# Kernel tuning notes

Measured on AMD Instinct MI355X. Metric: run time of the kernel, lower is better.

Reference implementation:

```python
import jax, jax.numpy as jnp
import numpy as np

N_HEADS = 12

def setup_inputs() -> dict:
    key = jax.random.key(0)
    ks = jax.random.split(key, 3)
    B, C, T = 4, 768, 2048
    x = jax.random.normal(ks[0], (B, C, T), dtype=jnp.float32)
    mask = jnp.ones((B, 1, 1, T), dtype=jnp.int32)  # all valid; masked_fill where mask==0
    Wqkv = jax.random.normal(ks[1], (3 * C, C), dtype=jnp.float32) * 0.02
    bqkv = jnp.zeros((3 * C,), dtype=jnp.float32)
    Wout = jax.random.normal(ks[2], (C, C), dtype=jnp.float32) * 0.02
    bout = jnp.zeros((C,), dtype=jnp.float32)
    return {"x": x, "mask": mask, "Wqkv": Wqkv, "bqkv": bqkv, "Wout": Wout, "bout": bout}


def reference(x, mask, Wqkv, bqkv, Wout, bout):
    B, C, T = x.shape
    H = N_HEADS
    d = C // H
    scale = 1.0 / jnp.sqrt(jnp.asarray(d, x.dtype))
    # 1x1 Conv1d == per-timestep matmul over channels
    qkv = jnp.einsum('oc,bct->bot', Wqkv, x) + bqkv[None, :, None]  # [B,3C,T]
    # channel dim splits as [3, H, d] per the torch view(B,3,H,d,T)
    qkv = qkv.reshape(B, 3, H, d, T).transpose(0, 1, 2, 4, 3)       # [B,3,H,T,d]
    q, k, v = qkv[:, 0], qkv[:, 1], qkv[:, 2]
    score = jnp.einsum('bhtd,bhsd->bhts', q, k) * scale             # [B,H,T,T]
    score = jnp.where(mask == 0, jnp.asarray(-10000.0, score.dtype), score)
    attn = jax.nn.softmax(score, axis=-1)  # dropout: eval mode (identity)
    o = jnp.einsum('bhts,bhsd->bhtd', attn, v)                      # [B,H,T,d]
    o = o.transpose(0, 1, 3, 2).reshape(B, C, T)                    # [B,C,T]
    return jnp.einsum('oc,bct->bot', Wout, o) + bout[None, :, None]
```

## Files before the change

kernel.cpp:

```cpp
#include <hip/hip_runtime.h>
#include <hip/hip_bf16.h>
#include <stdint.h>

#define B_   4
#define C_   768
#define T_   2048
#define H_   12
#define D_   64
#define O3_  2304

typedef __attribute__((ext_vector_type(4))) float f32x4;
typedef __attribute__((ext_vector_type(8))) short bf16x8;

__device__ __forceinline__ unsigned short f2bf(float f) {
  union { float f; unsigned int u; } v; v.f = f;
  unsigned int r = v.u + 0x7fffu + ((v.u >> 16) & 1u);
  return (unsigned short)(r >> 16);
}

__device__ __forceinline__ unsigned int pack2bf(float a, float b) {
  __hip_bfloat162 h2 = __float22bfloat162_rn(make_float2(a, b));
  union { __hip_bfloat162 h; unsigned int u; } cv; cv.h = h2;
  return cv.u;
}

__device__ __forceinline__ float fexp2(float x) {
#if __has_builtin(__builtin_amdgcn_exp2f)
  return __builtin_amdgcn_exp2f(x);
#else
  return exp2f(x);
#endif
}

__device__ __forceinline__ void async16(const void* g, void* lds) {
#if __has_builtin(__builtin_amdgcn_global_load_lds)
  __builtin_amdgcn_global_load_lds((const __attribute__((address_space(1))) void*)g,
                                   (__attribute__((address_space(3))) void*)lds, 16, 0, 0);
#else
  int lane = threadIdx.x & 63;
  *((uint4*)((char*)lds + lane * 16)) = *((const uint4*)g);
#endif
}


__global__ void cvt_f32_bf16(const float* __restrict__ in,
                             unsigned short* __restrict__ out, int n4) {
  int i = blockIdx.x * 256 + threadIdx.x;
  if (i < n4) {
    float4 f = ((const float4*)in)[i];
    ushort4 o;
    o.x = f2bf(f.x); o.y = f2bf(f.y); o.z = f2bf(f.z); o.w = f2bf(f.w);
    ((ushort4*)out)[i] = o;
  }
}

__global__ void make_bias(const int* __restrict__ mask, float* __restrict__ mbias, int n) {
  int i = blockIdx.x * 256 + threadIdx.x;
  if (i < n) mbias[i] = (mask[i] == 0) ? -14426.950408f : 0.0f;
}

__global__ void transpose_x(const float* __restrict__ x,
                            unsigned short* __restrict__ xT) {
  __shared__ unsigned short tile[32][33];
  int b = blockIdx.z;
  int c0 = blockIdx.y * 32;
  int t0 = blockIdx.x * 32;
  int tid = threadIdx.x;
  {
    int cl = tid >> 3;
    int tl = (tid & 7) * 4;
    float4 f = *(const float4*)(x + ((size_t)b * C_ + c0 + cl) * T_ + t0 + tl);
    tile[tl + 0][cl] = f2bf(f.x);
    tile[tl + 1][cl] = f2bf(f.y);
    tile[tl + 2][cl] = f2bf(f.z);
    tile[tl + 3][cl] = f2bf(f.w);
  }
  __syncthreads();
  {
    int tl = tid >> 3;
    int cl = (tid & 7) * 4;
    ushort4 o;
    o.x = tile[tl][cl + 0]; o.y = tile[tl][cl + 1];
    o.z = tile[tl][cl + 2]; o.w = tile[tl][cl + 3];
    *(ushort4*)(xT + ((size_t)b * T_ + t0 + tl) * C_ + c0 + cl) = o;
  }
}

__global__ __launch_bounds__(256)
void gemm_qkv(const unsigned short* __restrict__ xT,
              const unsigned short* __restrict__ W1,
              const float* __restrict__ bqkv,
              unsigned short* __restrict__ Qb,
              unsigned short* __restrict__ Kb,
              unsigned short* __restrict__ Vb) {
  __shared__ unsigned short sA[2][128 * 32];
  __shared__ unsigned short sB[2][128 * 32];

  const int b   = blockIdx.z;
  const int o0  = blockIdx.y * 128;
  const int t0  = blockIdx.x * 128;
  const int tid = threadIdx.x;
  const int wave = tid >> 6, lane = tid & 63;
  const int q = lane >> 4, ln = lane & 15;
  const int tw = wave >> 1, ow = wave & 1;

  const unsigned short* Ax = xT + (size_t)b * T_ * C_;
  const int srow = lane >> 2;
  const int scol = (lane & 3) * 8;

  const f32x4 ZERO = {0.f, 0.f, 0.f, 0.f};
  f32x4 acc[4][4];
#pragma unroll
  for (int mi = 0; mi < 4; ++mi)
#pragma unroll
    for (int ni = 0; ni < 4; ++ni) acc[mi][ni] = ZERO;

#pragma unroll
  for (int j = 0; j < 2; ++j) {
    const int chunk = wave * 2 + j;
    const int row = chunk * 16 + srow;
    async16(Ax + (size_t)(t0 + row) * C_ + scol, &sA[0][chunk * 512]);
    async16(W1 + (size_t)(o0 + row) * C_ + scol, &sB[0][chunk * 512]);
  }

  for (int i = 0; i < 24; ++i) {
    const int buf = i & 1;
    __syncthreads();
    if (i < 23) {
      const int k0 = (i + 1) * 32;
#pragma unroll
      for (int j = 0; j < 2; ++j) {
        const int chunk = wave * 2 + j;
        const int row = chunk * 16 + srow;
        async16(Ax + (size_t)(t0 + row) * C_ + k0 + scol, &sA[buf ^ 1][chunk * 512]);
        async16(W1 + (size_t)(o0 + row) * C_ + k0 + scol, &sB[buf ^ 1][chunk * 512]);
      }
    }

    bf16x8 aF[4], bF[4];
#pragma unroll
    for (int mi = 0; mi < 4; ++mi)
      aF[mi] = *(const bf16x8*)(&sA[buf][(tw * 64 + mi * 16 + ln) * 32 + q * 8]);
#pragma unroll
    for (int ni = 0; ni < 4; ++ni)
      bF[ni] = *(const bf16x8*)(&sB[buf][(ow * 64 + ni * 16 + ln) * 32 + q * 8]);
#pragma unroll
    for (int mi = 0; mi < 4; ++mi)
#pragma unroll
      for (int ni = 0; ni < 4; ++ni)
        acc[mi][ni] = __builtin_amdgcn_mfma_f32_16x16x32_bf16(aF[mi], bF[ni], acc[mi][ni], 0, 0, 0);
  }

  const float QSCL = 0.125f * 1.44269504f;
#pragma unroll
  for (int ni = 0; ni < 4; ++ni) {
    const int o = o0 + ow * 64 + ni * 16 + ln;
    const float bias = bqkv[o];
    const int which = o / C_;
    const int rem = o - which * C_;
    const int bh = b * H_ + (rem >> 6);
    const int dd = rem & 63;
#pragma unroll
    for (int mi = 0; mi < 4; ++mi) {
      const int tb = t0 + tw * 64 + mi * 16 + q * 4;
      f32x4 v = acc[mi][ni];
      if (which == 0) {
#pragma unroll
        for (int r = 0; r < 4; ++r)
          Qb[((size_t)bh * T_ + tb + r) * D_ + dd] = f2bf((v[r] + bias) * QSCL);
      } else if (which == 1) {
#pragma unroll
        for (int r = 0; r < 4; ++r) {
          const int s = tb + r;
          const int cp = (dd >> 3) ^ (s & 7);
          Kb[((size_t)bh * T_ + s) * 64 + (cp << 3) + (dd & 7)] = f2bf(v[r] + bias);
        }
      } else {
        const int tile = tb >> 6, si = tb & 63;
        const int cp = (si >> 3) ^ (dd & 7);
        ushort4 pk;
        pk.x = f2bf(v[0] + bias);
        pk.y = f2bf(v[1] + bias);
        pk.z = f2bf(v[2] + bias);
        pk.w = f2bf(v[3] + bias);
        *(ushort4*)(Vb + (((size_t)bh * 32 + tile) * 64 + dd) * 64 + (cp << 3) + (si & 7)) = pk;
      }
    }
  }
}

__global__ __launch_bounds__(128, 2)
void attn(const unsigned short* __restrict__ Qb,
          const unsigned short* __restrict__ Kb,
          const unsigned short* __restrict__ Vb,
          const float* __restrict__ mbias,
          unsigned short* __restrict__ Ob) {
  __shared__ unsigned short sK[2][64 * 64];
  __shared__ unsigned short sV[2][64 * 64];
  __shared__ unsigned short sP[2][64 * 80];

  const int id = blockIdx.x;
  const int bh = id % 48;
  const int tblk = id / 48;
  const int b = bh / H_, h = bh % H_;
  const int tid = threadIdx.x, wave = tid >> 6, lane = tid & 63;
  const int q = lane >> 4, ln = lane & 15;
  const int t0w = tblk * 128 + wave * 64;
  unsigned short* sPw = &sP[wave][0];

  bf16x8 Qa[4][2];
#pragma unroll
  for (int tt = 0; tt < 4; ++tt) {
    const unsigned short* qrow = Qb + ((size_t)bh * T_ + t0w + tt * 16 + ln) * D_;
    Qa[tt][0] = *(const bf16x8*)(qrow + q * 8);
    Qa[tt][1] = *(const bf16x8*)(qrow + 32 + q * 8);
  }

  const f32x4 ZERO = {0.f, 0.f, 0.f, 0.f};
  f32x4 Oacc[4][4];
  f32x4 lacc[4];
#pragma unroll
  for (int dt = 0; dt < 4; ++dt)
#pragma unroll
    for (int tt = 0; tt < 4; ++tt) Oacc[dt][tt] = ZERO;
#pragma unroll
  for (int tt = 0; tt < 4; ++tt) lacc[tt] = ZERO;

  const short one_s = (ln == 0) ? (short)0x3F80 : (short)0;
  bf16x8 ones;
#pragma unroll
  for (int j = 0; j < 8; ++j) ones[j] = one_s;

  const unsigned short* gK = Kb + (size_t)bh * T_ * 64;
  const unsigned short* gV = Vb + (size_t)bh * 32 * 4096;

#pragma unroll
  for (int j = 0; j < 4; ++j) {
    const int chunk = j * 2 + wave;
    async16(gK + chunk * 512 + lane * 8, &sK[0][chunk * 512]);
    async16(gV + chunk * 512 + lane * 8, &sV[0][chunk * 512]);
  }

  for (int it = 0; it < 32; ++it) {
    const int buf = it & 1;
    __syncthreads();
    if (it < 31) {
      const unsigned short* k = gK + (it + 1) * 4096;
      const unsigned short* v = gV + (it + 1) * 4096;
#pragma unroll
      for (int j = 0; j < 4; ++j) {
        const int chunk = j * 2 + wave;
        async16(k + chunk * 512 + lane * 8, &sK[buf ^ 1][chunk * 512]);
        async16(v + chunk * 512 + lane * 8, &sV[buf ^ 1][chunk * 512]);
      }
    }

    const int s0 = it * 64;
    const float bvl = mbias[b * T_ + s0 + lane];
    const bool anymask = (__ballot(bvl != 0.0f) != 0ull);
    const unsigned short* sKc = &sK[buf][0];
    const unsigned short* sVc = &sV[buf][0];

#pragma unroll
    for (int sb = 0; sb < 4; ++sb) {
      const unsigned short* krow = sKc + (sb * 16 + ln) * 64;
      bf16x8 kf0 = *(const bf16x8*)(krow + ((q ^ (ln & 7)) << 3));
      bf16x8 kf1 = *(const bf16x8*)(krow + (((4 + q) ^ (ln & 7)) << 3));
      f32x4 bb = ZERO;
      if (anymask) bb = *(const f32x4*)(mbias + b * T_ + s0 + sb * 16 + q * 4);
#pragma unroll
      for (int tt = 0; tt < 4; ++tt) {
        f32x4 p0 = __builtin_amdgcn_mfma_f32_16x16x32_bf16(kf0, Qa[tt][0], ZERO, 0, 0, 0);
        f32x4 sc = __builtin_amdgcn_mfma_f32_16x16x32_bf16(kf1, Qa[tt][1], p0, 0, 0, 0);
        if (anymask) {
#pragma unroll
          for (int r = 0; r < 4; ++r) sc[r] += bb[r];
        }
        uint2 w;
        w.x = pack2bf(fexp2(sc[0]), fexp2(sc[1]));
        w.y = pack2bf(fexp2(sc[2]), fexp2(sc[3]));
        *(uint2*)(sPw + (tt * 16 + ln) * 80 + sb * 16 + q * 4) = w;
      }
    }

#pragma unroll
    for (int c = 0; c < 2; ++c) {
      bf16x8 vf[4];
#pragma unroll
      for (int dt = 0; dt < 4; ++dt)
        vf[dt] = *(const bf16x8*)(sVc + (dt * 16 + ln) * 64 +
                                  (((c * 4 + q) ^ (ln & 7)) << 3));
#pragma unroll
      for (int tt = 0; tt < 4; ++tt) {
        bf16x8 pf = *(const bf16x8*)(sPw + (tt * 16 + ln) * 80 + c * 32 + q * 8);
        lacc[tt] = __builtin_amdgcn_mfma_f32_16x16x32_bf16(ones, pf, lacc[tt], 0, 0, 0);
#pragma unroll
        for (int dt = 0; dt < 4; ++dt)
          Oacc[dt][tt] = __builtin_amdgcn_mfma_f32_16x16x32_bf16(vf[dt], pf, Oacc[dt][tt], 0, 0, 0);
      }
    }
  }

#pragma unroll
  for (int tt = 0; tt < 4; ++tt) {
    const float lv = __shfl(lacc[tt][0], ln, 64);
    const float inv = 1.0f / lv;
    const int t = t0w + tt * 16 + ln;
#pragma unroll
    for (int dt = 0; dt < 4; ++dt) {
      ushort4 pk;
      pk.x = f2bf(Oacc[dt][tt][0] * inv);
      pk.y = f2bf(Oacc[dt][tt][1] * inv);
      pk.z = f2bf(Oacc[dt][tt][2] * inv);
      pk.w = f2bf(Oacc[dt][tt][3] * inv);
      *(ushort4*)(Ob + ((size_t)b * T_ + t) * C_ + h * D_ + dt * 16 + q * 4) = pk;
    }
  }
}

__global__ __launch_bounds__(256)
void gemm_out(const unsigned short* __restrict__ Ob,
              const unsigned short* __restrict__ W2,
              const float* __restrict__ bout,
              float* __restrict__ out) {
  __shared__ unsigned short sA[2][128 * 32];
  __shared__ unsigned short sB[2][128 * 32];

  const int b   = blockIdx.z;
  const int o0  = blockIdx.y * 128;
  const int t0  = blockIdx.x * 128;
  const int tid = threadIdx.x;
  const int wave = tid >> 6, lane = tid & 63;
  const int q = lane >> 4, ln = lane & 15;
  const int tw = wave >> 1, ow = wave & 1;

  const unsigned short* Bo = Ob + (size_t)b * T_ * C_;
  const int srow = lane >> 2;
  const int scol = (lane & 3) * 8;

  const f32x4 ZERO = {0.f, 0.f, 0.f, 0.f};
  f32x4 acc[4][4];
#pragma unroll
  for (int mi = 0; mi < 4; ++mi)
#pragma unroll
    for (int ni = 0; ni < 4; ++ni) acc[mi][ni] = ZERO;

#pragma unroll
  for (int j = 0; j < 2; ++j) {
    const int chunk = wave * 2 + j;
    const int row = chunk * 16 + srow;
    async16(W2 + (size_t)(o0 + row) * C_ + scol, &sA[0][chunk * 512]);
    async16(Bo + (size_t)(t0 + row) * C_ + scol, &sB[0][chunk * 512]);
  }

  for (int i = 0; i < 24; ++i) {
    const int buf = i & 1;
    __syncthreads();
    if (i < 23) {
      const int k0 = (i + 1) * 32;
#pragma unroll
      for (int j = 0; j < 2; ++j) {
        const int chunk = wave * 2 + j;
        const int row = chunk * 16 + srow;
        async16(W2 + (size_t)(o0 + row) * C_ + k0 + scol, &sA[buf ^ 1][chunk * 512]);
        async16(Bo + (size_t)(t0 + row) * C_ + k0 + scol, &sB[buf ^ 1][chunk * 512]);
      }
    }

    bf16x8 aF[4], bF[4];
#pragma unroll
    for (int mi = 0; mi < 4; ++mi)
      aF[mi] = *(const bf16x8*)(&sA[buf][(tw * 64 + mi * 16 + ln) * 32 + q * 8]);
#pragma unroll
    for (int ni = 0; ni < 4; ++ni)
      bF[ni] = *(const bf16x8*)(&sB[buf][(ow * 64 + ni * 16 + ln) * 32 + q * 8]);
#pragma unroll
    for (int mi = 0; mi < 4; ++mi)
#pragma unroll
      for (int ni = 0; ni < 4; ++ni)
        acc[mi][ni] = __builtin_amdgcn_mfma_f32_16x16x32_bf16(aF[mi], bF[ni], acc[mi][ni], 0, 0, 0);
  }

#pragma unroll
  for (int mi = 0; mi < 4; ++mi) {
    const int ob = o0 + tw * 64 + mi * 16 + q * 4;
#pragma unroll
    for (int ni = 0; ni < 4; ++ni) {
      const int t = t0 + ow * 64 + ni * 16 + ln;
      f32x4 v = acc[mi][ni];
#pragma unroll
      for (int r = 0; r < 4; ++r)
        out[((size_t)b * C_ + ob + r) * T_ + t] = v[r] + bout[ob + r];
    }
  }
}


extern "C" void kernel_launch(void* const* d_in, const int* in_sizes, int n_in,
                              void* d_out, int out_size, void* d_ws, size_t ws_size,
                              hipStream_t stream) {
  (void)in_sizes; (void)n_in; (void)out_size; (void)ws_size;
  const float* x    = (const float*)d_in[0];
  const int*   mask = (const int*)d_in[1];
  const float* Wqkv = (const float*)d_in[2];
  const float* bqkv = (const float*)d_in[3];
  const float* Wout = (const float*)d_in[4];
  const float* bout = (const float*)d_in[5];
  float* out = (float*)d_out;

  const size_t szHead = (size_t)B_ * H_ * T_ * D_;
  const size_t szBTC  = (size_t)B_ * T_ * C_;
  unsigned short* Qb  = (unsigned short*)d_ws;
  unsigned short* Kb  = Qb + szHead;
  unsigned short* Vb  = Kb + szHead;
  unsigned short* Ob  = Vb + szHead;
  unsigned short* xT  = Ob + szBTC;
  unsigned short* W1b = xT + szBTC;
  unsigned short* W2b = W1b + (size_t)O3_ * C_;
  float* mbias        = (float*)(W2b + (size_t)C_ * C_);

  cvt_f32_bf16<<<dim3((O3_ * C_ / 4 + 255) / 256), 256, 0, stream>>>(Wqkv, W1b, O3_ * C_ / 4);
  cvt_f32_bf16<<<dim3((C_ * C_ / 4 + 255) / 256), 256, 0, stream>>>(Wout, W2b, C_ * C_ / 4);
  make_bias<<<dim3((B_ * T_ + 255) / 256), 256, 0, stream>>>(mask, mbias, B_ * T_);
  transpose_x<<<dim3(T_ / 32, C_ / 32, B_), 256, 0, stream>>>(x, xT);
  gemm_qkv<<<dim3(T_ / 128, O3_ / 128, B_), 256, 0, stream>>>(xT, W1b, bqkv, Qb, Kb, Vb);
  attn<<<dim3(768), 128, 0, stream>>>(Qb, Kb, Vb, mbias, Ob);
  gemm_out<<<dim3(T_ / 128, C_ / 128, B_), 256, 0, stream>>>(Ob, W2b, bout, out);
}
```

Before: 257.4 us.

## Split attention key blocks across two wave pairs and reduce partial outputs

After: 238.0 us. -7.5%, faster.

```diff
diff --git a/kernel.cpp b/kernel.cpp
--- a/kernel.cpp
+++ b/kernel.cpp
@@ -189,15 +189,15 @@
   }
 }
 
-__global__ __launch_bounds__(128, 2)
+__global__ __launch_bounds__(256, 3)
 void attn(const unsigned short* __restrict__ Qb,
           const unsigned short* __restrict__ Kb,
           const unsigned short* __restrict__ Vb,
           const float* __restrict__ mbias,
           unsigned short* __restrict__ Ob) {
-  __shared__ unsigned short sK[2][64 * 64];
-  __shared__ unsigned short sV[2][64 * 64];
-  __shared__ unsigned short sP[2][64 * 80];
+  __shared__ __align__(16) char smem[53248];
+  unsigned short* sK0 = (unsigned short*)smem;
+  unsigned short* sV0 = (unsigned short*)(smem + 16384);
 
   const int id = blockIdx.x;
   const int bh = id % 48;
@@ -205,8 +205,9 @@
   const int b = bh / H_, h = bh % H_;
   const int tid = threadIdx.x, wave = tid >> 6, lane = tid & 63;
   const int q = lane >> 4, ln = lane & 15;
-  const int t0w = tblk * 128 + wave * 64;
-  unsigned short* sPw = &sP[wave][0];
+  const int wj = wave & 1, si = wave >> 1;
+  const int t0w = tblk * 128 + wj * 64;
+  unsigned short* sPw = (unsigned short*)(smem + 32768 + wave * 5120);
 
   bf16x8 Qa[4][2];
 #pragma unroll
@@ -235,10 +236,10 @@
   const unsigned short* gV = Vb + (size_t)bh * 32 * 4096;
 
 #pragma unroll
-  for (int j = 0; j < 4; ++j) {
-    const int chunk = j * 2 + wave;
-    async16(gK + chunk * 512 + lane * 8, &sK[0][chunk * 512]);
-    async16(gV + chunk * 512 + lane * 8, &sV[0][chunk * 512]);
+  for (int j = 0; j < 2; ++j) {
+    const int chunk = wave * 2 + j;
+    async16(gK + chunk * 512 + lane * 8, sK0 + chunk * 512);
+    async16(gV + chunk * 512 + lane * 8, sV0 + chunk * 512);
   }
 
   for (int it = 0; it < 32; ++it) {
@@ -247,27 +248,29 @@
     if (it < 31) {
       const unsigned short* k = gK + (it + 1) * 4096;
       const unsigned short* v = gV + (it + 1) * 4096;
-#pragma unroll
-      for (int j = 0; j < 4; ++j) {
-        const int chunk = j * 2 + wave;
-        async16(k + chunk * 512 + lane * 8, &sK[buf ^ 1][chunk * 512]);
-        async16(v + chunk * 512 + lane * 8, &sV[buf ^ 1][chunk * 512]);
+      unsigned short* dK = sK0 + (buf ^ 1) * 4096;
+      unsigned short* dV = sV0 + (buf ^ 1) * 4096;
+#pragma unroll
+      for (int j = 0; j < 2; ++j) {
+        const int chunk = wave * 2 + j;
+        async16(k + chunk * 512 + lane * 8, dK + chunk * 512);
+        async16(v + chunk * 512 + lane * 8, dV + chunk * 512);
       }
     }
 
     const int s0 = it * 64;
     const float bvl = mbias[b * T_ + s0 + lane];
     const bool anymask = (__ballot(bvl != 0.0f) != 0ull);
-    const unsigned short* sKc = &sK[buf][0];
-    const unsigned short* sVc = &sV[buf][0];
-
-#pragma unroll
-    for (int sb = 0; sb < 4; ++sb) {
-      const unsigned short* krow = sKc + (sb * 16 + ln) * 64;
+    const unsigned short* sKc = sK0 + buf * 4096;
+    const unsigned short* sVc = sV0 + buf * 4096;
+
+#pragma unroll
+    for (int sb = 0; sb < 2; ++sb) {
+      const unsigned short* krow = sKc + (si * 32 + sb * 16 + ln) * 64;
       bf16x8 kf0 = *(const bf16x8*)(krow + ((q ^ (ln & 7)) << 3));
       bf16x8 kf1 = *(const bf16x8*)(krow + (((4 + q) ^ (ln & 7)) << 3));
       f32x4 bb = ZERO;
-      if (anymask) bb = *(const f32x4*)(mbias + b * T_ + s0 + sb * 16 + q * 4);
+      if (anymask) bb = *(const f32x4*)(mbias + b * T_ + s0 + si * 32 + sb * 16 + q * 4);
 #pragma unroll
       for (int tt = 0; tt < 4; ++tt) {
         f32x4 p0 = __builtin_amdgcn_mfma_f32_16x16x32_bf16(kf0, Qa[tt][0], ZERO, 0, 0, 0);
@@ -279,41 +282,55 @@
         uint2 w;
         w.x = pack2bf(fexp2(sc[0]), fexp2(sc[1]));
         w.y = pack2bf(fexp2(sc[2]), fexp2(sc[3]));
-        *(uint2*)(sPw + (tt * 16 + ln) * 80 + sb * 16 + q * 4) = w;
-      }
-    }
-
-#pragma unroll
-    for (int c = 0; c < 2; ++c) {
-      bf16x8 vf[4];
+        *(uint2*)(sPw + (tt * 16 + ln) * 40 + sb * 16 + q * 4) = w;
+      }
+    }
+
+    bf16x8 vf[4];
+#pragma unroll
+    for (int dt = 0; dt < 4; ++dt)
+      vf[dt] = *(const bf16x8*)(sVc + (dt * 16 + ln) * 64 +
+                                (((si * 4 + q) ^ (ln & 7)) << 3));
+#pragma unroll
+    for (int tt = 0; tt < 4; ++tt) {
+      bf16x8 pf = *(const bf16x8*)(sPw + (tt * 16 + ln) * 40 + q * 8);
+      lacc[tt] = __builtin_amdgcn_mfma_f32_16x16x32_bf16(ones, pf, lacc[tt], 0, 0, 0);
 #pragma unroll
       for (int dt = 0; dt < 4; ++dt)
-        vf[dt] = *(const bf16x8*)(sVc + (dt * 16 + ln) * 64 +
-                                  (((c * 4 + q) ^ (ln & 7)) << 3));
-#pragma unroll
-      for (int tt = 0; tt < 4; ++tt) {
-        bf16x8 pf = *(const bf16x8*)(sPw + (tt * 16 + ln) * 80 + c * 32 + q * 8);
-        lacc[tt] = __builtin_amdgcn_mfma_f32_16x16x32_bf16(ones, pf, lacc[tt], 0, 0, 0);
-#pragma unroll
-        for (int dt = 0; dt < 4; ++dt)
-          Oacc[dt][tt] = __builtin_amdgcn_mfma_f32_16x16x32_bf16(vf[dt], pf, Oacc[dt][tt], 0, 0, 0);
-      }
-    }
-  }
-
-#pragma unroll
-  for (int tt = 0; tt < 4; ++tt) {
-    const float lv = __shfl(lacc[tt][0], ln, 64);
-    const float inv = 1.0f / lv;
-    const int t = t0w + tt * 16 + ln;
-#pragma unroll
-    for (int dt = 0; dt < 4; ++dt) {
-      ushort4 pk;
-      pk.x = f2bf(Oacc[dt][tt][0] * inv);
-      pk.y = f2bf(Oacc[dt][tt][1] * inv);
-      pk.z = f2bf(Oacc[dt][tt][2] * inv);
-      pk.w = f2bf(Oacc[dt][tt][3] * inv);
-      *(ushort4*)(Ob + ((size_t)b * T_ + t) * C_ + h * D_ + dt * 16 + q * 4) = pk;
+        Oacc[dt][tt] = __builtin_amdgcn_mfma_f32_16x16x32_bf16(vf[dt], pf, Oacc[dt][tt], 0, 0, 0);
+    }
+  }
+
+  __syncthreads();
+  float* fbuf = (float*)smem;
+  float* lbuf = (float*)(smem + 34816);
+  if (si == 1) {
+#pragma unroll
+    for (int tt = 0; tt < 4; ++tt) {
+#pragma unroll
+      for (int dt = 0; dt < 4; ++dt)
+        *(f32x4*)(fbuf + ((size_t)(wj * 64 + tt * 16 + ln)) * 68 + dt * 16 + q * 4) = Oacc[dt][tt];
+      if (q == 0) lbuf[wj * 64 + tt * 16 + ln] = lacc[tt][0];
+    }
+  }
+  __syncthreads();
+  if (si == 0) {
+#pragma unroll
+    for (int tt = 0; tt < 4; ++tt) {
+      const float lv = __shfl(lacc[tt][0], ln, 64) + lbuf[wj * 64 + tt * 16 + ln];
+      const float inv = 1.0f / lv;
+      const int t = t0w + tt * 16 + ln;
+#pragma unroll
+      for (int dt = 0; dt < 4; ++dt) {
+        f32x4 o = Oacc[dt][tt];
+        f32x4 p = *(const f32x4*)(fbuf + ((size_t)(wj * 64 + tt * 16 + ln)) * 68 + dt * 16 + q * 4);
+        ushort4 pk;
+        pk.x = f2bf((o[0] + p[0]) * inv);
+        pk.y = f2bf((o[1] + p[1]) * inv);
+        pk.z = f2bf((o[2] + p[2]) * inv);
+        pk.w = f2bf((o[3] + p[3]) * inv);
+        *(ushort4*)(Ob + ((size_t)b * T_ + t) * C_ + h * D_ + dt * 16 + q * 4) = pk;
+      }
     }
   }
 }
@@ -424,6 +441,6 @@
   make_bias<<<dim3((B_ * T_ + 255) / 256), 256, 0, stream>>>(mask, mbias, B_ * T_);
   transpose_x<<<dim3(T_ / 32, C_ / 32, B_), 256, 0, stream>>>(x, xT);
   gemm_qkv<<<dim3(T_ / 128, O3_ / 128, B_), 256, 0, stream>>>(xT, W1b, bqkv, Qb, Kb, Vb);
-  attn<<<dim3(768), 128, 0, stream>>>(Qb, Kb, Vb, mbias, Ob);
+  attn<<<dim3(768), 256, 0, stream>>>(Qb, Kb, Vb, mbias, Ob);
   gemm_out<<<dim3(T_ / 128, C_ / 128, B_), 256, 0, stream>>>(Ob, W2b, bout, out);
 }
```
